# Optimization experiments

Hardware: AMD Instinct MI355X
Metric: run time of the kernel (lower is better)

Reference implementation:

```python
import jax, jax.numpy as jnp
import numpy as np

N, D_IN = 16384, 3
HID = 1024
R, K = 64, 64
NQ = 4096

def _glorot(key, fan_in, fan_out):
    lim = np.sqrt(6.0 / (fan_in + fan_out)).astype(np.float32)
    return jax.random.uniform(key, (fan_in, fan_out), jnp.float32, -lim, lim)

def setup_inputs() -> dict:
    key = jax.random.key(0)
    ks = jax.random.split(key, 12)
    return {
        "input": jax.random.normal(ks[0], (N, D_IN), jnp.float32),
        "eq_param": jax.random.uniform(ks[1], (1,), jnp.float32),
        "quad_x0": jax.random.uniform(ks[2], (NQ, D_IN), jnp.float32),
        "quad_x1": jax.random.uniform(ks[3], (NQ, D_IN), jnp.float32),
        # mlp_x: D_IN -> HID -> R*R
        "Wx1": _glorot(ks[4], D_IN, HID), "bx1": jnp.zeros((HID,), jnp.float32),
        "Wx2": _glorot(ks[5], HID, R * R), "bx2": jnp.zeros((R * R,), jnp.float32),
        # mlp_quad[0]: D_IN -> HID -> R*K
        "Wq0a": _glorot(ks[6], D_IN, HID), "bq0a": jnp.zeros((HID,), jnp.float32),
        "Wq0b": _glorot(ks[7], HID, R * K), "bq0b": jnp.zeros((R * K,), jnp.float32),
        # mlp_quad[1]: D_IN -> HID -> R*K
        "Wq1a": _glorot(ks[8], D_IN, HID), "bq1a": jnp.zeros((HID,), jnp.float32),
        "Wq1b": _glorot(ks[9], HID, R * K), "bq1b": jnp.zeros((R * K,), jnp.float32),
    }

def _mlp(x, W1, b1, W2, b2):
    return jnp.tanh(x @ W1 + b1) @ W2 + b2

def reference(input, eq_param, quad_x0, quad_x1,
              Wx1, bx1, Wx2, bx2,
              Wq0a, bq0a, Wq0b, bq0b,
              Wq1a, bq1a, Wq1b, bq1b):
    # r_func: Gaussian quadrature weights y_i = exp(-eq_param * ||q||^2), shape [n_i, 1]
    y0 = jnp.exp(-eq_param * jnp.sum(quad_x0 * quad_x0, axis=1, keepdims=True))
    y1 = jnp.exp(-eq_param * jnp.sum(quad_x1 * quad_x1, axis=1, keepdims=True))
    lhs = _mlp(input, Wx1, bx1, Wx2, bx2)                        # [N, R*R]
    q0 = (y0 * _mlp(quad_x0, Wq0a, bq0a, Wq0b, bq0b)).reshape(-1, R, K)  # [n0, R, K]
    q1 = (y1 * _mlp(quad_x1, Wq1a, bq1a, Wq1b, bq1b)).reshape(-1, R, K)  # [n1, R, K]
    # rhs[b,d] = sum_{a,c,x} q0[a,b,x] q1[c,d,x]
    #          = sum_x (sum_a q0[a,b,x]) (sum_c q1[c,d,x])
    # Algebraically identical to the original einsum('abx,cdx->abcd') -> movedim -> sum(0),
    # without materializing the O(n0*R*n1*R) tensor.
    S0 = q0.sum(axis=0)                                          # [R, K]
    S1 = q1.sum(axis=0)                                          # [R, K]
    rhs = S0 @ S1.T                                              # [R, R] (b, d)
    return lhs @ rhs.reshape(-1)                                 # [N]
```

## Files before the change

kernel.cpp:

```cpp
#include <hip/hip_runtime.h>

#define OFF_U0   0
#define OFF_U1   1024
#define OFF_SY   2048
#define OFF_S0   2052
#define OFF_S1   6148
#define OFF_RHS  10244
#define OFF_W2R  14340
#define OFF_C    15364
#define MEMSET_FLOATS 10244

__device__ __forceinline__ float tanh_fast(float x) {
    float e = __expf(x + x);
    return 1.0f - 2.0f * __builtin_amdgcn_rcpf(e + 1.0f);
}

__global__ __launch_bounds__(256) void k1(
    const float* __restrict__ qx0, const float* __restrict__ qx1,
    const float* __restrict__ Wa0, const float* __restrict__ Wa1,
    const float* __restrict__ ba0, const float* __restrict__ ba1,
    const float* __restrict__ eqp, float* __restrict__ ws, int achunks)
{
    int bx = blockIdx.x;
    int s  = bx / achunks;
    int ac = bx - s * achunks;
    const float* qx = s ? qx1 : qx0;
    const float* Wa = s ? Wa1 : Wa0;
    const float* ba = s ? ba1 : ba0;
    float* u   = ws + (s ? OFF_U1 : OFF_U0);
    float* syp = ws + OFF_SY + s;

    __shared__ float qL[64][3];
    __shared__ float yL[64];

    int tid = threadIdx.x;
    float eq = eqp[0];
    float my_y = 0.0f;
    if (tid < 64) {
        int a = ac * 64 + tid;
        float q0 = qx[a*3+0], q1 = qx[a*3+1], q2 = qx[a*3+2];
        qL[tid][0] = q0; qL[tid][1] = q1; qL[tid][2] = q2;
        my_y = __expf(-eq * (q0*q0 + q1*q1 + q2*q2));
        yL[tid] = my_y;
    }
    __syncthreads();

    float w0[4], w1[4], w2[4], bb[4], acc[4];
    #pragma unroll
    for (int k = 0; k < 4; ++k) {
        int h = tid + 256*k;
        w0[k] = Wa[h];
        w1[k] = Wa[1024 + h];
        w2[k] = Wa[2048 + h];
        bb[k] = ba[h];
        acc[k] = 0.0f;
    }
    for (int a = 0; a < 64; ++a) {
        float q0 = qL[a][0], q1 = qL[a][1], q2 = qL[a][2];
        float ya = yL[a];
        #pragma unroll
        for (int k = 0; k < 4; ++k) {
            float z = fmaf(q0, w0[k], fmaf(q1, w1[k], fmaf(q2, w2[k], bb[k])));
            acc[k] = fmaf(ya, tanh_fast(z), acc[k]);
        }
    }
    #pragma unroll
    for (int k = 0; k < 4; ++k)
        atomicAdd(&u[tid + 256*k], acc[k]);

    if (tid < 64) {
        float v = my_y;
        #pragma unroll
        for (int off = 32; off > 0; off >>= 1)
            v += __shfl_down(v, off);
        if (tid == 0) atomicAdd(syp, v);
    }
}

__global__ __launch_bounds__(256) void k2(
    const float* __restrict__ Wb0, const float* __restrict__ Wb1,
    const float* __restrict__ bb0, const float* __restrict__ bb1,
    float* __restrict__ ws)
{
    int bx = blockIdx.x;
    int s  = bx >> 7;
    int r  = bx & 127;
    int hc = r >> 2;
    int jc = r & 3;
    const float* Wb = s ? Wb1 : Wb0;
    const float* bb = s ? bb1 : bb0;
    const float* u  = ws + (s ? OFF_U1 : OFF_U0) + hc * 32;
    float* S = ws + (s ? OFF_S1 : OFF_S0);
    float sy = ws[OFF_SY + s];

    __shared__ float uL[32];
    int tid = threadIdx.x;
    if (tid < 32) uL[tid] = u[tid];
    __syncthreads();

    int j = jc * 1024 + tid * 4;
    float4 acc;
    if (hc == 0) {
        float4 b4 = *reinterpret_cast<const float4*>(bb + j);
        acc = make_float4(sy*b4.x, sy*b4.y, sy*b4.z, sy*b4.w);
    } else {
        acc = make_float4(0.f, 0.f, 0.f, 0.f);
    }

    const float* row = Wb + (hc * 32) * 4096 + j;
    #pragma unroll 8
    for (int h = 0; h < 32; ++h) {
        float4 w = *reinterpret_cast<const float4*>(row);
        float uh = uL[h];
        acc.x = fmaf(uh, w.x, acc.x);
        acc.y = fmaf(uh, w.y, acc.y);
        acc.z = fmaf(uh, w.z, acc.z);
        acc.w = fmaf(uh, w.w, acc.w);
        row += 4096;
    }
    atomicAdd(&S[j+0], acc.x);
    atomicAdd(&S[j+1], acc.y);
    atomicAdd(&S[j+2], acc.z);
    atomicAdd(&S[j+3], acc.w);
}

__global__ __launch_bounds__(256) void k3(float* __restrict__ ws)
{
    __shared__ float S0L[4096];
    __shared__ float S1T[64 * 65];
    const float* S0 = ws + OFF_S0;
    const float* S1 = ws + OFF_S1;
    float* rhs = ws + OFF_RHS;
    int tid = threadIdx.x;
    for (int i = tid; i < 4096; i += 256) {
        S0L[i] = S0[i];
        int d = i >> 6, x = i & 63;
        S1T[x * 65 + d] = S1[i];
    }
    __syncthreads();
    int o = blockIdx.x * 256 + tid;
    int b = o >> 6, d = o & 63;
    float acc = 0.0f;
    #pragma unroll 8
    for (int x = 0; x < 64; ++x)
        acc = fmaf(S0L[b*64 + x], S1T[x*65 + d], acc);
    rhs[o] = acc;
}

__global__ __launch_bounds__(256) void k4(
    const float* __restrict__ Wx2, const float* __restrict__ bx2,
    float* __restrict__ ws)
{
    __shared__ float4 rhsL[1024];
    const float4* rhs4 = reinterpret_cast<const float4*>(ws + OFF_RHS);
    int tid = threadIdx.x;
    for (int i = tid; i < 1024; i += 256) rhsL[i] = rhs4[i];
    __syncthreads();
    int wave = tid >> 6, lane = tid & 63;
    int rowIdx = blockIdx.x * 4 + wave;
    if (rowIdx > 1024) return;
    const float4* src4 = reinterpret_cast<const float4*>(
        (rowIdx < 1024) ? (Wx2 + rowIdx * 4096) : bx2);
    float acc = 0.0f;
    #pragma unroll
    for (int i = 0; i < 16; ++i) {
        float4 w = src4[lane + 64*i];
        float4 rv = rhsL[lane + 64*i];
        acc += w.x*rv.x + w.y*rv.y + w.z*rv.z + w.w*rv.w;
    }
    #pragma unroll
    for (int off = 32; off > 0; off >>= 1)
        acc += __shfl_down(acc, off);
    if (lane == 0) {
        if (rowIdx < 1024) ws[OFF_W2R + rowIdx] = acc;
        else               ws[OFF_C] = acc;
    }
}

__global__ __launch_bounds__(256) void k5(
    const float* __restrict__ input, const float* __restrict__ Wx1,
    const float* __restrict__ bx1, const float* __restrict__ ws,
    float* __restrict__ out, int N)
{
    __shared__ float4 WL[1024];
    __shared__ float w2rL[1024];
    int tid = threadIdx.x;
    #pragma unroll
    for (int k = 0; k < 4; ++k) {
        int h = tid + 256*k;
        WL[h] = make_float4(Wx1[h], Wx1[1024 + h], Wx1[2048 + h], bx1[h]);
        w2rL[h] = ws[OFF_W2R + h];
    }
    __syncthreads();
    int n = blockIdx.x * 64 + (tid >> 2);
    int p = tid & 3;
    int nc = (n < N) ? n : (N - 1);
    float in0 = input[nc*3+0], in1 = input[nc*3+1], in2 = input[nc*3+2];
    float acc = 0.0f;
    #pragma unroll 4
    for (int i = 0; i < 256; ++i) {
        int h = 4*i + p;
        float4 w = WL[h];
        float z = fmaf(in0, w.x, fmaf(in1, w.y, fmaf(in2, w.z, w.w)));
        acc = fmaf(tanh_fast(z), w2rL[h], acc);
    }
    acc += __shfl_xor(acc, 1);
    acc += __shfl_xor(acc, 2);
    if (p == 0 && n < N) out[n] = acc + ws[OFF_C];
}

extern "C" void kernel_launch(void* const* d_in, const int* in_sizes, int n_in,
                              void* d_out, int out_size, void* d_ws, size_t ws_size,
                              hipStream_t stream)
{
    const float* input = (const float*)d_in[0];
    const float* eqp   = (const float*)d_in[1];
    const float* qx0   = (const float*)d_in[2];
    const float* qx1   = (const float*)d_in[3];
    const float* Wx1   = (const float*)d_in[4];
    const float* bx1   = (const float*)d_in[5];
    const float* Wx2   = (const float*)d_in[6];
    const float* bx2   = (const float*)d_in[7];
    const float* Wq0a  = (const float*)d_in[8];
    const float* bq0a  = (const float*)d_in[9];
    const float* Wq0b  = (const float*)d_in[10];
    const float* bq0b  = (const float*)d_in[11];
    const float* Wq1a  = (const float*)d_in[12];
    const float* bq1a  = (const float*)d_in[13];
    const float* Wq1b  = (const float*)d_in[14];
    const float* bq1b  = (const float*)d_in[15];
    float* ws  = (float*)d_ws;
    float* out = (float*)d_out;

    int N  = in_sizes[0] / 3;
    int NQ = in_sizes[2] / 3;
    int achunks = NQ / 64;

    hipMemsetAsync(d_ws, 0, MEMSET_FLOATS * sizeof(float), stream);
    hipLaunchKernelGGL(k1, dim3(2 * achunks), dim3(256), 0, stream,
                       qx0, qx1, Wq0a, Wq1a, bq0a, bq1a, eqp, ws, achunks);
    hipLaunchKernelGGL(k2, dim3(256), dim3(256), 0, stream,
                       Wq0b, Wq1b, bq0b, bq1b, ws);
    hipLaunchKernelGGL(k3, dim3(16), dim3(256), 0, stream, ws);
    hipLaunchKernelGGL(k4, dim3(257), dim3(256), 0, stream, Wx2, bx2, ws);
    hipLaunchKernelGGL(k5, dim3((N + 63) / 64), dim3(256), 0, stream,
                       input, Wx1, bx1, ws, out, N);
}
```

Before: 145.6 us.

## Fuse five kernels into one cooperative persistent kernel with grid syncs

Replaces the memset plus five separate launches with a single cooperative kernel of 256 blocks that uses grid.sync between stages. Atomic accumulation of the hidden sums is replaced by per-block partial buffers that are reduced in the next stage. Every block now recomputes the 64x64 rhs matrix redundantly in shared memory instead of a separate k3 launch. This removes launch gaps and the memset, at the cost of grid-wide barrier overhead and redundant rhs work.

```diff
diff --git a/kernel.cpp b/kernel.cpp
--- a/kernel.cpp
+++ b/kernel.cpp
@@ -1,212 +1,221 @@
 #include <hip/hip_runtime.h>
-
-#define OFF_U0   0
-#define OFF_U1   1024
-#define OFF_SY   2048
-#define OFF_S0   2052
-#define OFF_S1   6148
-#define OFF_RHS  10244
-#define OFF_W2R  14340
-#define OFF_C    15364
-#define MEMSET_FLOATS 10244
+#include <hip/hip_cooperative_groups.h>
+
+namespace cg = cooperative_groups;
+
+#define OFF_PART_U   0
+#define OFF_PART_SY  262144
+#define OFF_S        262400
+#define OFF_W2R      270592
+#define OFF_C        271616
 
 __device__ __forceinline__ float tanh_fast(float x) {
     float e = __expf(x + x);
     return 1.0f - 2.0f * __builtin_amdgcn_rcpf(e + 1.0f);
 }
 
-__global__ __launch_bounds__(256) void k1(
+union SharedU {
+    struct { float qL[32][3]; float yL[32]; } a;
+    struct { float uRed[8][32]; float syL; } b;
+    struct { float S0L[4096]; float S1T[64*65]; float rhsL[4096]; } cd;
+    struct { float4 WL[1024]; float w2rL[1024]; } e;
+};
+
+__global__ __launch_bounds__(256, 1) void fused(
+    const float* __restrict__ input,
+    const float* __restrict__ eqp,
     const float* __restrict__ qx0, const float* __restrict__ qx1,
-    const float* __restrict__ Wa0, const float* __restrict__ Wa1,
-    const float* __restrict__ ba0, const float* __restrict__ ba1,
-    const float* __restrict__ eqp, float* __restrict__ ws, int achunks)
+    const float* __restrict__ Wx1, const float* __restrict__ bx1,
+    const float* __restrict__ Wx2, const float* __restrict__ bx2,
+    const float* __restrict__ Wq0a, const float* __restrict__ bq0a,
+    const float* __restrict__ Wq0b, const float* __restrict__ bq0b,
+    const float* __restrict__ Wq1a, const float* __restrict__ bq1a,
+    const float* __restrict__ Wq1b, const float* __restrict__ bq1b,
+    float* __restrict__ ws, float* __restrict__ out, int N, int NQ)
 {
-    int bx = blockIdx.x;
-    int s  = bx / achunks;
-    int ac = bx - s * achunks;
-    const float* qx = s ? qx1 : qx0;
-    const float* Wa = s ? Wa1 : Wa0;
-    const float* ba = s ? ba1 : ba0;
-    float* u   = ws + (s ? OFF_U1 : OFF_U0);
-    float* syp = ws + OFF_SY + s;
-
-    __shared__ float qL[64][3];
-    __shared__ float yL[64];
-
-    int tid = threadIdx.x;
-    float eq = eqp[0];
-    float my_y = 0.0f;
-    if (tid < 64) {
-        int a = ac * 64 + tid;
-        float q0 = qx[a*3+0], q1 = qx[a*3+1], q2 = qx[a*3+2];
-        qL[tid][0] = q0; qL[tid][1] = q1; qL[tid][2] = q2;
-        my_y = __expf(-eq * (q0*q0 + q1*q1 + q2*q2));
-        yL[tid] = my_y;
-    }
-    __syncthreads();
-
-    float w0[4], w1[4], w2[4], bb[4], acc[4];
-    #pragma unroll
-    for (int k = 0; k < 4; ++k) {
-        int h = tid + 256*k;
-        w0[k] = Wa[h];
-        w1[k] = Wa[1024 + h];
-        w2[k] = Wa[2048 + h];
-        bb[k] = ba[h];
-        acc[k] = 0.0f;
-    }
-    for (int a = 0; a < 64; ++a) {
-        float q0 = qL[a][0], q1 = qL[a][1], q2 = qL[a][2];
-        float ya = yL[a];
+    cg::grid_group grid = cg::this_grid();
+    __shared__ SharedU sh;
+    const int b = blockIdx.x, tid = threadIdx.x;
+    const int s = b >> 7, chunk = b & 127;
+
+    if (tid < 32) ws[OFF_S + b * 32 + tid] = 0.0f;
+
+    {
+        const int PPB = NQ / 128;
+        const float* qx = s ? qx1 : qx0;
+        const float* Wa = s ? Wq1a : Wq0a;
+        const float* ba = s ? bq1a : bq0a;
+        float eq = eqp[0];
+        float my_y = 0.0f;
+        if (tid < PPB) {
+            int a = chunk * PPB + tid;
+            float q0 = qx[a*3+0], q1 = qx[a*3+1], q2 = qx[a*3+2];
+            sh.a.qL[tid][0] = q0; sh.a.qL[tid][1] = q1; sh.a.qL[tid][2] = q2;
+            my_y = __expf(-eq * (q0*q0 + q1*q1 + q2*q2));
+            sh.a.yL[tid] = my_y;
+        }
+        __syncthreads();
+        float w0[4], w1[4], w2[4], bb4[4], acc[4];
         #pragma unroll
         for (int k = 0; k < 4; ++k) {
-            float z = fmaf(q0, w0[k], fmaf(q1, w1[k], fmaf(q2, w2[k], bb[k])));
-            acc[k] = fmaf(ya, tanh_fast(z), acc[k]);
-        }
-    }
-    #pragma unroll
-    for (int k = 0; k < 4; ++k)
-        atomicAdd(&u[tid + 256*k], acc[k]);
-
-    if (tid < 64) {
-        float v = my_y;
-        #pragma unroll
-        for (int off = 32; off > 0; off >>= 1)
-            v += __shfl_down(v, off);
-        if (tid == 0) atomicAdd(syp, v);
-    }
-}
-
-__global__ __launch_bounds__(256) void k2(
-    const float* __restrict__ Wb0, const float* __restrict__ Wb1,
-    const float* __restrict__ bb0, const float* __restrict__ bb1,
-    float* __restrict__ ws)
-{
-    int bx = blockIdx.x;
-    int s  = bx >> 7;
-    int r  = bx & 127;
-    int hc = r >> 2;
-    int jc = r & 3;
-    const float* Wb = s ? Wb1 : Wb0;
-    const float* bb = s ? bb1 : bb0;
-    const float* u  = ws + (s ? OFF_U1 : OFF_U0) + hc * 32;
-    float* S = ws + (s ? OFF_S1 : OFF_S0);
-    float sy = ws[OFF_SY + s];
-
-    __shared__ float uL[32];
-    int tid = threadIdx.x;
-    if (tid < 32) uL[tid] = u[tid];
-    __syncthreads();
-
-    int j = jc * 1024 + tid * 4;
-    float4 acc;
-    if (hc == 0) {
-        float4 b4 = *reinterpret_cast<const float4*>(bb + j);
-        acc = make_float4(sy*b4.x, sy*b4.y, sy*b4.z, sy*b4.w);
-    } else {
-        acc = make_float4(0.f, 0.f, 0.f, 0.f);
-    }
-
-    const float* row = Wb + (hc * 32) * 4096 + j;
-    #pragma unroll 8
-    for (int h = 0; h < 32; ++h) {
-        float4 w = *reinterpret_cast<const float4*>(row);
-        float uh = uL[h];
-        acc.x = fmaf(uh, w.x, acc.x);
-        acc.y = fmaf(uh, w.y, acc.y);
-        acc.z = fmaf(uh, w.z, acc.z);
-        acc.w = fmaf(uh, w.w, acc.w);
-        row += 4096;
-    }
-    atomicAdd(&S[j+0], acc.x);
-    atomicAdd(&S[j+1], acc.y);
-    atomicAdd(&S[j+2], acc.z);
-    atomicAdd(&S[j+3], acc.w);
-}
-
-__global__ __launch_bounds__(256) void k3(float* __restrict__ ws)
-{
-    __shared__ float S0L[4096];
-    __shared__ float S1T[64 * 65];
-    const float* S0 = ws + OFF_S0;
-    const float* S1 = ws + OFF_S1;
-    float* rhs = ws + OFF_RHS;
-    int tid = threadIdx.x;
-    for (int i = tid; i < 4096; i += 256) {
-        S0L[i] = S0[i];
-        int d = i >> 6, x = i & 63;
-        S1T[x * 65 + d] = S1[i];
-    }
-    __syncthreads();
-    int o = blockIdx.x * 256 + tid;
-    int b = o >> 6, d = o & 63;
-    float acc = 0.0f;
-    #pragma unroll 8
-    for (int x = 0; x < 64; ++x)
-        acc = fmaf(S0L[b*64 + x], S1T[x*65 + d], acc);
-    rhs[o] = acc;
-}
-
-__global__ __launch_bounds__(256) void k4(
-    const float* __restrict__ Wx2, const float* __restrict__ bx2,
-    float* __restrict__ ws)
-{
-    __shared__ float4 rhsL[1024];
-    const float4* rhs4 = reinterpret_cast<const float4*>(ws + OFF_RHS);
-    int tid = threadIdx.x;
-    for (int i = tid; i < 1024; i += 256) rhsL[i] = rhs4[i];
-    __syncthreads();
-    int wave = tid >> 6, lane = tid & 63;
-    int rowIdx = blockIdx.x * 4 + wave;
-    if (rowIdx > 1024) return;
-    const float4* src4 = reinterpret_cast<const float4*>(
-        (rowIdx < 1024) ? (Wx2 + rowIdx * 4096) : bx2);
-    float acc = 0.0f;
-    #pragma unroll
-    for (int i = 0; i < 16; ++i) {
-        float4 w = src4[lane + 64*i];
-        float4 rv = rhsL[lane + 64*i];
-        acc += w.x*rv.x + w.y*rv.y + w.z*rv.z + w.w*rv.w;
-    }
-    #pragma unroll
-    for (int off = 32; off > 0; off >>= 1)
-        acc += __shfl_down(acc, off);
-    if (lane == 0) {
-        if (rowIdx < 1024) ws[OFF_W2R + rowIdx] = acc;
-        else               ws[OFF_C] = acc;
-    }
-}
-
-__global__ __launch_bounds__(256) void k5(
-    const float* __restrict__ input, const float* __restrict__ Wx1,
-    const float* __restrict__ bx1, const float* __restrict__ ws,
-    float* __restrict__ out, int N)
-{
-    __shared__ float4 WL[1024];
-    __shared__ float w2rL[1024];
-    int tid = threadIdx.x;
-    #pragma unroll
-    for (int k = 0; k < 4; ++k) {
-        int h = tid + 256*k;
-        WL[h] = make_float4(Wx1[h], Wx1[1024 + h], Wx1[2048 + h], bx1[h]);
-        w2rL[h] = ws[OFF_W2R + h];
-    }
-    __syncthreads();
-    int n = blockIdx.x * 64 + (tid >> 2);
-    int p = tid & 3;
-    int nc = (n < N) ? n : (N - 1);
-    float in0 = input[nc*3+0], in1 = input[nc*3+1], in2 = input[nc*3+2];
-    float acc = 0.0f;
-    #pragma unroll 4
-    for (int i = 0; i < 256; ++i) {
-        int h = 4*i + p;
-        float4 w = WL[h];
-        float z = fmaf(in0, w.x, fmaf(in1, w.y, fmaf(in2, w.z, w.w)));
-        acc = fmaf(tanh_fast(z), w2rL[h], acc);
-    }
-    acc += __shfl_xor(acc, 1);
-    acc += __shfl_xor(acc, 2);
-    if (p == 0 && n < N) out[n] = acc + ws[OFF_C];
+            int h = tid + 256*k;
+            w0[k] = Wa[h]; w1[k] = Wa[1024+h]; w2[k] = Wa[2048+h];
+            bb4[k] = ba[h]; acc[k] = 0.0f;
+        }
+        for (int a = 0; a < PPB; ++a) {
+            float q0 = sh.a.qL[a][0], q1 = sh.a.qL[a][1], q2 = sh.a.qL[a][2];
+            float ya = sh.a.yL[a];
+            #pragma unroll
+            for (int k = 0; k < 4; ++k) {
+                float z = fmaf(q0, w0[k], fmaf(q1, w1[k], fmaf(q2, w2[k], bb4[k])));
+                acc[k] = fmaf(ya, tanh_fast(z), acc[k]);
+            }
+        }
+        #pragma unroll
+        for (int k = 0; k < 4; ++k)
+            ws[OFF_PART_U + b*1024 + tid + 256*k] = acc[k];
+        if (tid < 32) {
+            float v = my_y;
+            #pragma unroll
+            for (int off = 16; off > 0; off >>= 1) v += __shfl_down(v, off);
+            if (tid == 0) ws[OFF_PART_SY + b] = v;
+        }
+    }
+
+    grid.sync();
+
+    {
+        int r = b & 127, hc = r >> 2, jc = r & 3;
+        const float* Wb = s ? Wq1b : Wq0b;
+        const float* bb = s ? bq1b : bq0b;
+        int hl = tid & 31, pg = tid >> 5;
+        float accu = 0.0f;
+        #pragma unroll 4
+        for (int p = pg*16; p < pg*16 + 16; ++p)
+            accu += ws[OFF_PART_U + (s*128 + p)*1024 + hc*32 + hl];
+        sh.b.uRed[pg][hl] = accu;
+        float sv = 0.0f;
+        if (tid < 64)
+            sv = ws[OFF_PART_SY + s*128 + tid] + ws[OFF_PART_SY + s*128 + 64 + tid];
+        __syncthreads();
+        if (tid < 32) {
+            float t = 0.0f;
+            #pragma unroll
+            for (int g = 0; g < 8; ++g) t += sh.b.uRed[g][tid];
+            sh.b.uRed[0][tid] = t;
+        }
+        if (tid < 64) {
+            #pragma unroll
+            for (int off = 32; off > 0; off >>= 1) sv += __shfl_down(sv, off);
+            if (tid == 0) sh.b.syL = sv;
+        }
+        __syncthreads();
+        float sy = sh.b.syL;
+        int j = jc * 1024 + tid * 4;
+        float4 acc;
+        if (hc == 0) {
+            float4 b4 = *reinterpret_cast<const float4*>(bb + j);
+            acc = make_float4(sy*b4.x, sy*b4.y, sy*b4.z, sy*b4.w);
+        } else {
+            acc = make_float4(0.f, 0.f, 0.f, 0.f);
+        }
+        const float* row = Wb + (hc*32)*4096 + j;
+        #pragma unroll 8
+        for (int h = 0; h < 32; ++h) {
+            float4 w = *reinterpret_cast<const float4*>(row);
+            float uh = sh.b.uRed[0][h];
+            acc.x = fmaf(uh, w.x, acc.x);
+            acc.y = fmaf(uh, w.y, acc.y);
+            acc.z = fmaf(uh, w.z, acc.z);
+            acc.w = fmaf(uh, w.w, acc.w);
+            row += 4096;
+        }
+        float* S = ws + OFF_S + s * 4096;
+        atomicAdd(&S[j+0], acc.x);
+        atomicAdd(&S[j+1], acc.y);
+        atomicAdd(&S[j+2], acc.z);
+        atomicAdd(&S[j+3], acc.w);
+    }
+
+    grid.sync();
+
+    {
+        const float* S = ws + OFF_S;
+        for (int i = tid; i < 4096; i += 256) {
+            sh.cd.S0L[i] = S[i];
+            int d = i >> 6, x = i & 63;
+            sh.cd.S1T[x*65 + d] = S[4096 + i];
+        }
+        __syncthreads();
+        #pragma unroll
+        for (int k = 0; k < 16; ++k) {
+            int o = k*256 + tid;
+            int br = o >> 6, d = o & 63;
+            float acc = 0.0f;
+            #pragma unroll 8
+            for (int x = 0; x < 64; ++x)
+                acc = fmaf(sh.cd.S0L[br*64 + x], sh.cd.S1T[x*65 + d], acc);
+            sh.cd.rhsL[o] = acc;
+        }
+        __syncthreads();
+        int wave = tid >> 6, lane = tid & 63;
+        int rowIdx = b*4 + wave;
+        const float4* rhs4 = reinterpret_cast<const float4*>(sh.cd.rhsL);
+        {
+            const float4* src4 = reinterpret_cast<const float4*>(Wx2 + rowIdx*4096);
+            float acc = 0.0f;
+            #pragma unroll
+            for (int i = 0; i < 16; ++i) {
+                float4 w  = src4[lane + 64*i];
+                float4 rv = rhs4[lane + 64*i];
+                acc += w.x*rv.x + w.y*rv.y + w.z*rv.z + w.w*rv.w;
+            }
+            #pragma unroll
+            for (int off = 32; off > 0; off >>= 1) acc += __shfl_down(acc, off);
+            if (lane == 0) ws[OFF_W2R + rowIdx] = acc;
+        }
+        if (b == 0 && wave == 0) {
+            const float4* src4 = reinterpret_cast<const float4*>(bx2);
+            float acc = 0.0f;
+            #pragma unroll
+            for (int i = 0; i < 16; ++i) {
+                float4 w  = src4[lane + 64*i];
+                float4 rv = rhs4[lane + 64*i];
+                acc += w.x*rv.x + w.y*rv.y + w.z*rv.z + w.w*rv.w;
+            }
+            #pragma unroll
+            for (int off = 32; off > 0; off >>= 1) acc += __shfl_down(acc, off);
+            if (lane == 0) ws[OFF_C] = acc;
+        }
+    }
+
+    grid.sync();
+
+    {
+        #pragma unroll
+        for (int k = 0; k < 4; ++k) {
+            int h = tid + 256*k;
+            sh.e.WL[h] = make_float4(Wx1[h], Wx1[1024+h], Wx1[2048+h], bx1[h]);
+            sh.e.w2rL[h] = ws[OFF_W2R + h];
+        }
+        __syncthreads();
+        float c = ws[OFF_C];
+        int p = tid & 3;
+        for (int n = b*64 + (tid >> 2); n < N; n += 256*64) {
+            float in0 = input[n*3+0], in1 = input[n*3+1], in2 = input[n*3+2];
+            float acc = 0.0f;
+            #pragma unroll 4
+            for (int i = 0; i < 256; ++i) {
+                int h = 4*i + p;
+                float4 w = sh.e.WL[h];
+                float z = fmaf(in0, w.x, fmaf(in1, w.y, fmaf(in2, w.z, w.w)));
+                acc = fmaf(tanh_fast(z), sh.e.w2rL[h], acc);
+            }
+            acc += __shfl_xor(acc, 1);
+            acc += __shfl_xor(acc, 2);
+            if (p == 0) out[n] = acc + c;
+        }
+    }
 }
 
 extern "C" void kernel_launch(void* const* d_in, const int* in_sizes, int n_in,
@@ -234,15 +243,13 @@
 
     int N  = in_sizes[0] / 3;
     int NQ = in_sizes[2] / 3;
-    int achunks = NQ / 64;
-
-    hipMemsetAsync(d_ws, 0, MEMSET_FLOATS * sizeof(float), stream);
-    hipLaunchKernelGGL(k1, dim3(2 * achunks), dim3(256), 0, stream,
-                       qx0, qx1, Wq0a, Wq1a, bq0a, bq1a, eqp, ws, achunks);
-    hipLaunchKernelGGL(k2, dim3(256), dim3(256), 0, stream,
-                       Wq0b, Wq1b, bq0b, bq1b, ws);
-    hipLaunchKernelGGL(k3, dim3(16), dim3(256), 0, stream, ws);
-    hipLaunchKernelGGL(k4, dim3(257), dim3(256), 0, stream, Wx2, bx2, ws);
-    hipLaunchKernelGGL(k5, dim3((N + 63) / 64), dim3(256), 0, stream,
-                       input, Wx1, bx1, ws, out, N);
+
+    void* args[] = {
+        (void*)&input, (void*)&eqp, (void*)&qx0, (void*)&qx1,
+        (void*)&Wx1, (void*)&bx1, (void*)&Wx2, (void*)&bx2,
+        (void*)&Wq0a, (void*)&bq0a, (void*)&Wq0b, (void*)&bq0b,
+        (void*)&Wq1a, (void*)&bq1a, (void*)&Wq1b, (void*)&bq1b,
+        (void*)&ws, (void*)&out, (void*)&N, (void*)&NQ
+    };
+    hipLaunchCooperativeKernel((void*)fused, dim3(256), dim3(256), args, 0, stream);
 }
```

Result: slower. 258.4 us (+77.5%).

## Replace atomics and memset with per-block partials, widen grids in k1 and k5

Applied to the files above, without the earlier changes.

k1 now runs 256 blocks of 32 quadrature points each and writes per-block partial sums of the hidden activations and weights to workspace instead of using atomicAdd. k2 reduces those partials itself, and k1 zeroes the S accumulators, so the hipMemsetAsync call is dropped. k5 now uses 8 threads per row and twice as many blocks to raise parallelism, and tanh uses exp2 with a prescaled argument. The trade is extra partial-sum traffic and redundant reduction work in every k2 block, in exchange for removing one memset launch and atomic contention. Zeroing S inside k1 relies on k1 completing before k2 on the same stream.

```diff
diff --git a/kernel.cpp b/kernel.cpp
--- a/kernel.cpp
+++ b/kernel.cpp
@@ -1,17 +1,14 @@
 #include <hip/hip_runtime.h>
 
-#define OFF_U0   0
-#define OFF_U1   1024
-#define OFF_SY   2048
-#define OFF_S0   2052
-#define OFF_S1   6148
-#define OFF_RHS  10244
-#define OFF_W2R  14340
-#define OFF_C    15364
-#define MEMSET_FLOATS 10244
+#define OFF_PART_U   0
+#define OFF_PART_SY  262144
+#define OFF_S        262400
+#define OFF_RHS      270592
+#define OFF_W2R      274688
+#define OFF_C        275712
 
 __device__ __forceinline__ float tanh_fast(float x) {
-    float e = __expf(x + x);
+    float e = __builtin_amdgcn_exp2f(x * 2.885390081777927f);
     return 1.0f - 2.0f * __builtin_amdgcn_rcpf(e + 1.0f);
 }
 
@@ -19,25 +16,24 @@
     const float* __restrict__ qx0, const float* __restrict__ qx1,
     const float* __restrict__ Wa0, const float* __restrict__ Wa1,
     const float* __restrict__ ba0, const float* __restrict__ ba1,
-    const float* __restrict__ eqp, float* __restrict__ ws, int achunks)
-{
-    int bx = blockIdx.x;
-    int s  = bx / achunks;
-    int ac = bx - s * achunks;
+    const float* __restrict__ eqp, float* __restrict__ ws, int NQ)
+{
+    const int b = blockIdx.x, tid = threadIdx.x;
+    const int s = b >> 7, chunk = b & 127;
+    const int PPB = NQ / 128;
     const float* qx = s ? qx1 : qx0;
     const float* Wa = s ? Wa1 : Wa0;
     const float* ba = s ? ba1 : ba0;
-    float* u   = ws + (s ? OFF_U1 : OFF_U0);
-    float* syp = ws + OFF_SY + s;
-
-    __shared__ float qL[64][3];
-    __shared__ float yL[64];
-
-    int tid = threadIdx.x;
+
+    __shared__ float qL[32][3];
+    __shared__ float yL[32];
+
+    if (tid < 32) ws[OFF_S + b*32 + tid] = 0.0f;
+
     float eq = eqp[0];
     float my_y = 0.0f;
-    if (tid < 64) {
-        int a = ac * 64 + tid;
+    if (tid < PPB) {
+        int a = chunk * PPB + tid;
         float q0 = qx[a*3+0], q1 = qx[a*3+1], q2 = qx[a*3+2];
         qL[tid][0] = q0; qL[tid][1] = q1; qL[tid][2] = q2;
         my_y = __expf(-eq * (q0*q0 + q1*q1 + q2*q2));
@@ -45,35 +41,31 @@
     }
     __syncthreads();
 
-    float w0[4], w1[4], w2[4], bb[4], acc[4];
+    float w0[4], w1[4], w2[4], bb4[4], acc[4];
     #pragma unroll
     for (int k = 0; k < 4; ++k) {
         int h = tid + 256*k;
-        w0[k] = Wa[h];
-        w1[k] = Wa[1024 + h];
-        w2[k] = Wa[2048 + h];
-        bb[k] = ba[h];
-        acc[k] = 0.0f;
-    }
-    for (int a = 0; a < 64; ++a) {
+        w0[k] = Wa[h]; w1[k] = Wa[1024+h]; w2[k] = Wa[2048+h];
+        bb4[k] = ba[h]; acc[k] = 0.0f;
+    }
+    for (int a = 0; a < PPB; ++a) {
         float q0 = qL[a][0], q1 = qL[a][1], q2 = qL[a][2];
         float ya = yL[a];
         #pragma unroll
         for (int k = 0; k < 4; ++k) {
-            float z = fmaf(q0, w0[k], fmaf(q1, w1[k], fmaf(q2, w2[k], bb[k])));
+            float z = fmaf(q0, w0[k], fmaf(q1, w1[k], fmaf(q2, w2[k], bb4[k])));
             acc[k] = fmaf(ya, tanh_fast(z), acc[k]);
         }
     }
     #pragma unroll
     for (int k = 0; k < 4; ++k)
-        atomicAdd(&u[tid + 256*k], acc[k]);
-
-    if (tid < 64) {
+        ws[OFF_PART_U + b*1024 + tid + 256*k] = acc[k];
+
+    if (tid < 32) {
         float v = my_y;
         #pragma unroll
-        for (int off = 32; off > 0; off >>= 1)
-            v += __shfl_down(v, off);
-        if (tid == 0) atomicAdd(syp, v);
+        for (int off = 16; off > 0; off >>= 1) v += __shfl_down(v, off);
+        if (tid == 0) ws[OFF_PART_SY + b] = v;
     }
 }
 
@@ -82,22 +74,39 @@
     const float* __restrict__ bb0, const float* __restrict__ bb1,
     float* __restrict__ ws)
 {
-    int bx = blockIdx.x;
-    int s  = bx >> 7;
-    int r  = bx & 127;
-    int hc = r >> 2;
-    int jc = r & 3;
+    const int bx = blockIdx.x, tid = threadIdx.x;
+    const int s = bx >> 7, r = bx & 127;
+    const int hc = r >> 2, jc = r & 3;
     const float* Wb = s ? Wb1 : Wb0;
     const float* bb = s ? bb1 : bb0;
-    const float* u  = ws + (s ? OFF_U1 : OFF_U0) + hc * 32;
-    float* S = ws + (s ? OFF_S1 : OFF_S0);
-    float sy = ws[OFF_SY + s];
-
-    __shared__ float uL[32];
-    int tid = threadIdx.x;
-    if (tid < 32) uL[tid] = u[tid];
-    __syncthreads();
-
+
+    __shared__ float uRed[8][32];
+    __shared__ float syL;
+
+    int hl = tid & 31, pg = tid >> 5;
+    float accu = 0.0f;
+    #pragma unroll 4
+    for (int p = pg*16; p < pg*16 + 16; ++p)
+        accu += ws[OFF_PART_U + (s*128 + p)*1024 + hc*32 + hl];
+    uRed[pg][hl] = accu;
+    float sv = 0.0f;
+    if (tid < 64)
+        sv = ws[OFF_PART_SY + s*128 + tid] + ws[OFF_PART_SY + s*128 + 64 + tid];
+    __syncthreads();
+    if (tid < 32) {
+        float t = 0.0f;
+        #pragma unroll
+        for (int g = 0; g < 8; ++g) t += uRed[g][tid];
+        uRed[0][tid] = t;
+    }
+    if (tid < 64) {
+        #pragma unroll
+        for (int off = 32; off > 0; off >>= 1) sv += __shfl_down(sv, off);
+        if (tid == 0) syL = sv;
+    }
+    __syncthreads();
+
+    float sy = syL;
     int j = jc * 1024 + tid * 4;
     float4 acc;
     if (hc == 0) {
@@ -106,18 +115,18 @@
     } else {
         acc = make_float4(0.f, 0.f, 0.f, 0.f);
     }
-
-    const float* row = Wb + (hc * 32) * 4096 + j;
+    const float* row = Wb + (hc*32)*4096 + j;
     #pragma unroll 8
     for (int h = 0; h < 32; ++h) {
         float4 w = *reinterpret_cast<const float4*>(row);
-        float uh = uL[h];
+        float uh = uRed[0][h];
         acc.x = fmaf(uh, w.x, acc.x);
         acc.y = fmaf(uh, w.y, acc.y);
         acc.z = fmaf(uh, w.z, acc.z);
         acc.w = fmaf(uh, w.w, acc.w);
         row += 4096;
     }
+    float* S = ws + OFF_S + s * 4096;
     atomicAdd(&S[j+0], acc.x);
     atomicAdd(&S[j+1], acc.y);
     atomicAdd(&S[j+2], acc.z);
@@ -128,8 +137,8 @@
 {
     __shared__ float S0L[4096];
     __shared__ float S1T[64 * 65];
-    const float* S0 = ws + OFF_S0;
-    const float* S1 = ws + OFF_S1;
+    const float* S0 = ws + OFF_S;
+    const float* S1 = ws + OFF_S + 4096;
     float* rhs = ws + OFF_RHS;
     int tid = threadIdx.x;
     for (int i = tid; i < 4096; i += 256) {
@@ -164,13 +173,12 @@
     float acc = 0.0f;
     #pragma unroll
     for (int i = 0; i < 16; ++i) {
-        float4 w = src4[lane + 64*i];
+        float4 w  = src4[lane + 64*i];
         float4 rv = rhsL[lane + 64*i];
         acc += w.x*rv.x + w.y*rv.y + w.z*rv.z + w.w*rv.w;
     }
     #pragma unroll
-    for (int off = 32; off > 0; off >>= 1)
-        acc += __shfl_down(acc, off);
+    for (int off = 32; off > 0; off >>= 1) acc += __shfl_down(acc, off);
     if (lane == 0) {
         if (rowIdx < 1024) ws[OFF_W2R + rowIdx] = acc;
         else               ws[OFF_C] = acc;
@@ -188,25 +196,27 @@
     #pragma unroll
     for (int k = 0; k < 4; ++k) {
         int h = tid + 256*k;
-        WL[h] = make_float4(Wx1[h], Wx1[1024 + h], Wx1[2048 + h], bx1[h]);
+        WL[h] = make_float4(Wx1[h], Wx1[1024+h], Wx1[2048+h], bx1[h]);
         w2rL[h] = ws[OFF_W2R + h];
     }
     __syncthreads();
-    int n = blockIdx.x * 64 + (tid >> 2);
-    int p = tid & 3;
+    float c = ws[OFF_C];
+    int n = blockIdx.x * 32 + (tid >> 3);
+    int p = tid & 7;
     int nc = (n < N) ? n : (N - 1);
     float in0 = input[nc*3+0], in1 = input[nc*3+1], in2 = input[nc*3+2];
     float acc = 0.0f;
     #pragma unroll 4
-    for (int i = 0; i < 256; ++i) {
-        int h = 4*i + p;
+    for (int i = 0; i < 128; ++i) {
+        int h = 8*i + p;
         float4 w = WL[h];
         float z = fmaf(in0, w.x, fmaf(in1, w.y, fmaf(in2, w.z, w.w)));
         acc = fmaf(tanh_fast(z), w2rL[h], acc);
     }
     acc += __shfl_xor(acc, 1);
     acc += __shfl_xor(acc, 2);
-    if (p == 0 && n < N) out[n] = acc + ws[OFF_C];
+    acc += __shfl_xor(acc, 4);
+    if (p == 0 && n < N) out[n] = acc + c;
 }
 
 extern "C" void kernel_launch(void* const* d_in, const int* in_sizes, int n_in,
@@ -234,15 +244,13 @@
 
     int N  = in_sizes[0] / 3;
     int NQ = in_sizes[2] / 3;
-    int achunks = NQ / 64;
-
-    hipMemsetAsync(d_ws, 0, MEMSET_FLOATS * sizeof(float), stream);
-    hipLaunchKernelGGL(k1, dim3(2 * achunks), dim3(256), 0, stream,
-                       qx0, qx1, Wq0a, Wq1a, bq0a, bq1a, eqp, ws, achunks);
+
+    hipLaunchKernelGGL(k1, dim3(256), dim3(256), 0, stream,
+                       qx0, qx1, Wq0a, Wq1a, bq0a, bq1a, eqp, ws, NQ);
     hipLaunchKernelGGL(k2, dim3(256), dim3(256), 0, stream,
                        Wq0b, Wq1b, bq0b, bq1b, ws);
     hipLaunchKernelGGL(k3, dim3(16), dim3(256), 0, stream, ws);
     hipLaunchKernelGGL(k4, dim3(257), dim3(256), 0, stream, Wx2, bx2, ws);
-    hipLaunchKernelGGL(k5, dim3((N + 63) / 64), dim3(256), 0, stream,
+    hipLaunchKernelGGL(k5, dim3((N + 31) / 32), dim3(256), 0, stream,
                        input, Wx1, bx1, ws, out, N);
 }
```

Measured after the change: 138.4 us, median of 2. 4.9% less time.
